# Optimization experiments

Hardware: AMD Instinct MI355X
Metric: run time of the kernel (lower is better)

Reference implementation:

```python
import jax, jax.numpy as jnp
import numpy as np

N_NODES = 100000
N_EDGES = 640000
NIN = 128
NOUT = 128


def setup_inputs() -> dict:
    key = jax.random.key(0)
    ks = jax.random.split(key, 10)
    scale = 1.0 / np.sqrt(NIN)
    x = jax.random.normal(ks[0], (N_NODES, NIN), dtype=jnp.float32)
    edge_index = jax.random.randint(ks[1], (2, N_EDGES), 0, N_NODES, dtype=jnp.int64)
    edge_attr = jnp.zeros((N_EDGES, 1), dtype=jnp.float32)
    Wk = jax.random.uniform(ks[2], (NIN, NOUT), jnp.float32, -scale, scale)
    bk = jax.random.uniform(ks[3], (NOUT,), jnp.float32, -scale, scale)
    Wq = jax.random.uniform(ks[4], (NIN, NOUT), jnp.float32, -scale, scale)
    bq = jax.random.uniform(ks[5], (NOUT,), jnp.float32, -scale, scale)
    Wv = jax.random.uniform(ks[6], (NIN, NOUT), jnp.float32, -scale, scale)
    bv = jax.random.uniform(ks[7], (NOUT,), jnp.float32, -scale, scale)
    Wskip = jax.random.uniform(ks[8], (NIN, NOUT), jnp.float32, -scale, scale)
    bias = jax.random.uniform(ks[9], (NOUT,), jnp.float32, -scale, scale)
    return {
        "x": x, "edge_index": edge_index, "edge_attr": edge_attr,
        "Wk": Wk, "bk": bk, "Wq": Wq, "bq": bq,
        "Wv": Wv, "bv": bv, "Wskip": Wskip, "bias": bias,
    }


def reference(x, edge_index, edge_attr, Wk, bk, Wq, bq, Wv, bv, Wskip, bias):
    # PyG ResGatedGraphConv: out_i = W_skip x_i + b + sum_{j->i} sigmoid(k_i + q_j) * v_j
    # k = lin_key(x) (applied to dst), q = lin_query(x) (src), v = lin_value(x) (src)
    src, dst = edge_index[0], edge_index[1]
    k = x @ Wk + bk            # [N, NOUT]
    q = x @ Wq + bq            # [N, NOUT]
    v = x @ Wv + bv            # [N, NOUT]
    eta = jax.nn.sigmoid(k[dst] + q[src])   # [E, NOUT] per-edge gate
    msg = eta * v[src]                       # [E, NOUT]
    agg = jax.ops.segment_sum(msg, dst, num_segments=x.shape[0])  # [N, NOUT]
    return agg + x @ Wskip + bias
```

## Files before the change

kernel.cpp:

```cpp
#include <hip/hip_runtime.h>
#include <hip/hip_bf16.h>

typedef __bf16 v4bf __attribute__((ext_vector_type(4)));
typedef __bf16 v8bf __attribute__((ext_vector_type(8)));
typedef float  v16f __attribute__((ext_vector_type(16)));

#define LOG2E 1.44269504088896340736f

__device__ __forceinline__ unsigned short f2bf(float f) {
    union { float f; unsigned int u; } a; a.f = f;
    unsigned int r = a.u + 0x7FFFu + ((a.u >> 16) & 1u);
    return (unsigned short)(r >> 16);
}

__device__ __forceinline__ void unpack8(uint4 rawv, float* f) {
    unsigned int w[4] = { rawv.x, rawv.y, rawv.z, rawv.w };
    #pragma unroll
    for (int i = 0; i < 4; ++i) {
        f[2 * i]     = __uint_as_float(w[i] << 16);
        f[2 * i + 1] = __uint_as_float(w[i] & 0xFFFF0000u);
    }
}

__global__ __launch_bounds__(256) void prep_w_zero(
    const float* __restrict__ Wk, const float* __restrict__ Wq,
    const float* __restrict__ Wv, const float* __restrict__ Ws,
    unsigned short* __restrict__ Wt, int* __restrict__ deg, int N)
{
    int i = blockIdx.x * 256 + threadIdx.x;
    if (i < 65536) {
        int m = i >> 14;
        int r = i & 16383;
        int n = r >> 7, k = r & 127;
        const float* W = (m == 0) ? Wk : (m == 1) ? Wq : (m == 2) ? Wv : Ws;
        float scale = (m < 2) ? LOG2E : 1.0f;
        Wt[i] = f2bf(W[k * 128 + n] * scale);
    }
    if (i < N) deg[i] = 0;
}

__global__ __launch_bounds__(1024, 4) void gemm_fused(
    const float* __restrict__ x, int N,
    const unsigned short* __restrict__ Wt,
    const float* __restrict__ bk, const float* __restrict__ bq,
    const float* __restrict__ bv, const float* __restrict__ bs,
    unsigned short* __restrict__ kws, unsigned short* __restrict__ qv,
    float* __restrict__ out)
{
    __shared__ __align__(16) unsigned short xs[32 * 132];
    const int t   = threadIdx.x;
    const int wid = t >> 6;
    const int m   = wid >> 2;
    const int ct  = wid & 3;
    const int l   = t & 63;
    const int col = ct * 32 + (l & 31);
    const int kb  = (l >> 5) * 8;

    v8bf b[8];
    {
        const unsigned short* wp = Wt + m * 16384 + col * 128 + kb;
        #pragma unroll
        for (int c = 0; c < 8; ++c) b[c] = *(const v8bf*)(wp + c * 16);
    }
    const float* bvec = (m == 0) ? bk : (m == 1) ? bq : (m == 2) ? bv : bs;
    const float bcol = bvec[col] * ((m < 2) ? LOG2E : 1.0f);
    unsigned short* dst; int dstride;
    if (m == 0)      { dst = kws;      dstride = 128; }
    else if (m == 1) { dst = qv;       dstride = 256; }
    else             { dst = qv + 128; dstride = 256; }

    const int srow = t >> 5;
    const int sk4  = (t & 31) << 2;
    const int rowb = 4 * (l >> 5);

    const int ntiles = (N + 31) >> 5;
    int tile = blockIdx.x;
    if (tile >= ntiles) return;

    float4 stg = make_float4(0.f, 0.f, 0.f, 0.f);
    {
        int gr = tile * 32 + srow;
        if (gr < N) stg = *(const float4*)(x + (size_t)gr * 128 + sk4);
    }

    const unsigned short* ap = xs + (l & 31) * 132 + kb;

    while (true) {
        ushort4 pk;
        pk.x = f2bf(stg.x); pk.y = f2bf(stg.y);
        pk.z = f2bf(stg.z); pk.w = f2bf(stg.w);
        *(ushort4*)(xs + srow * 132 + sk4) = pk;
        __syncthreads();

        int next = tile + gridDim.x;
        if (next < ntiles) {
            int gr = next * 32 + srow;
            stg = (gr < N) ? *(const float4*)(x + (size_t)gr * 128 + sk4)
                           : make_float4(0.f, 0.f, 0.f, 0.f);
        }

        v16f acc = {};
        #pragma unroll
        for (int c = 0; c < 8; ++c) {
            v4bf a0 = *(const v4bf*)(ap + c * 16);
            v4bf a1 = *(const v4bf*)(ap + c * 16 + 4);
            v8bf a = __builtin_shufflevector(a0, a1, 0, 1, 2, 3, 4, 5, 6, 7);
            acc = __builtin_amdgcn_mfma_f32_32x32x16_bf16(a, b[c], acc, 0, 0, 0);
        }

        const int r0 = tile * 32 + rowb;
        if (m == 3) {
            #pragma unroll
            for (int reg = 0; reg < 16; ++reg) {
                int row = r0 + (reg & 3) + 8 * (reg >> 2);
                if (row < N) out[(size_t)row * 128 + col] = acc[reg] + bcol;
            }
        } else {
            #pragma unroll
            for (int reg = 0; reg < 16; ++reg) {
                int row = r0 + (reg & 3) + 8 * (reg >> 2);
                if (row < N) dst[(size_t)row * dstride + col] = f2bf(acc[reg] + bcol);
            }
        }

        tile = next;
        if (tile >= ntiles) break;
        __syncthreads();
    }
}


__global__ __launch_bounds__(256) void count_deg(
    const int* __restrict__ ei, int E, int* __restrict__ deg)
{
    int e = blockIdx.x * 256 + threadIdx.x;
    if (e >= E) return;
    atomicAdd(&deg[ei[E + e]], 1);
}

__global__ __launch_bounds__(256) void scan_chunks(
    const int* __restrict__ deg, int N, int* __restrict__ rowStart,
    int* __restrict__ chunkTot)
{
    __shared__ int sums[256];
    const int t = threadIdx.x;
    const int base = blockIdx.x * 1024 + t * 4;
    int d0 = 0, d1 = 0, d2 = 0, d3 = 0;
    if (base + 3 < N) {
        int4 dd = *(const int4*)(deg + base);
        d0 = dd.x; d1 = dd.y; d2 = dd.z; d3 = dd.w;
    } else {
        if (base + 0 < N) d0 = deg[base + 0];
        if (base + 1 < N) d1 = deg[base + 1];
        if (base + 2 < N) d2 = deg[base + 2];
        if (base + 3 < N) d3 = deg[base + 3];
    }
    int tot = d0 + d1 + d2 + d3;
    sums[t] = tot;
    __syncthreads();
    #pragma unroll
    for (int off = 1; off < 256; off <<= 1) {
        int v = (t >= off) ? sums[t - off] : 0;
        __syncthreads();
        sums[t] += v;
        __syncthreads();
    }
    int excl = sums[t] - tot;
    if (base + 0 < N) rowStart[base + 0] = excl;
    if (base + 1 < N) rowStart[base + 1] = excl + d0;
    if (base + 2 < N) rowStart[base + 2] = excl + d0 + d1;
    if (base + 3 < N) rowStart[base + 3] = excl + d0 + d1 + d2;
    if (t == 255) chunkTot[blockIdx.x] = sums[255];
}

__global__ __launch_bounds__(256) void add_offsets(
    int* __restrict__ rowStart, int* __restrict__ rowEnd,
    const int* __restrict__ chunkTot, int N, int nChunks)
{
    __shared__ int s[128];
    const int t = threadIdx.x;
    if (t < 128) s[t] = (t < nChunks) ? chunkTot[t] : 0;
    __syncthreads();
    #pragma unroll
    for (int off = 1; off < 128; off <<= 1) {
        int u = 0;
        if (t < 128 && t >= off) u = s[t - off];
        __syncthreads();
        if (t < 128) s[t] += u;
        __syncthreads();
    }
    const int coff = (blockIdx.x == 0) ? 0 : s[blockIdx.x - 1];
    const int base = blockIdx.x * 1024 + t * 4;
    if (base + 3 < N) {
        int4 r = *(const int4*)(rowStart + base);
        r.x += coff; r.y += coff; r.z += coff; r.w += coff;
        *(int4*)(rowStart + base) = r;
        *(int4*)(rowEnd + base) = r;
    } else {
        #pragma unroll
        for (int j = 0; j < 4; ++j) {
            if (base + j < N) {
                int v = rowStart[base + j] + coff;
                rowStart[base + j] = v;
                rowEnd[base + j] = v;
            }
        }
    }
}

__global__ __launch_bounds__(256) void fill_csr(
    const int* __restrict__ ei, int E,
    int* __restrict__ rowEnd, int* __restrict__ elist)
{
    int e = blockIdx.x * 256 + threadIdx.x;
    if (e >= E) return;
    int s = ei[e];
    int d = ei[E + e];
    int pos = atomicAdd(&rowEnd[d], 1);
    elist[pos] = s;
}

__global__ __launch_bounds__(256) void gather_agg(
    const int* __restrict__ rowStart, const int* __restrict__ rowEnd,
    const int* __restrict__ elist,
    const unsigned short* __restrict__ kws,
    const unsigned short* __restrict__ qv,
    float* __restrict__ out, int N)
{
    int gid = blockIdx.x * 256 + threadIdx.x;
    int node = gid >> 4;
    if (node >= N) return;
    int fo = (gid & 15) << 3;

    uint4 kraw = *(const uint4*)(kws + (size_t)node * 128 + fo);
    kraw.x ^= 0x80008000u; kraw.y ^= 0x80008000u;
    kraw.z ^= 0x80008000u; kraw.w ^= 0x80008000u;
    float nkf[8];
    unpack8(kraw, nkf);
    float acc[8] = {};

    const unsigned short* qvb = qv + fo;
    int p = rowStart[node];
    const int e = rowEnd[node];

    for (; p + 4 <= e; p += 4) {
        int s0 = elist[p], s1 = elist[p + 1], s2 = elist[p + 2], s3 = elist[p + 3];
        const unsigned short* r0 = qvb + (size_t)s0 * 256;
        const unsigned short* r1 = qvb + (size_t)s1 * 256;
        const unsigned short* r2 = qvb + (size_t)s2 * 256;
        const unsigned short* r3 = qvb + (size_t)s3 * 256;
        uint4 q0r = *(const uint4*)(r0);
        uint4 v0r = *(const uint4*)(r0 + 128);
        uint4 q1r = *(const uint4*)(r1);
        uint4 v1r = *(const uint4*)(r1 + 128);
        uint4 q2r = *(const uint4*)(r2);
        uint4 v2r = *(const uint4*)(r2 + 128);
        uint4 q3r = *(const uint4*)(r3);
        uint4 v3r = *(const uint4*)(r3 + 128);
        float qf[8], vf[8];
        unpack8(q0r, qf); unpack8(v0r, vf);
        #pragma unroll
        for (int j = 0; j < 8; ++j) {
            float ex = __builtin_amdgcn_exp2f(nkf[j] - qf[j]);
            acc[j] = fmaf(__builtin_amdgcn_rcpf(1.0f + ex), vf[j], acc[j]);
        }
        unpack8(q1r, qf); unpack8(v1r, vf);
        #pragma unroll
        for (int j = 0; j < 8; ++j) {
            float ex = __builtin_amdgcn_exp2f(nkf[j] - qf[j]);
            acc[j] = fmaf(__builtin_amdgcn_rcpf(1.0f + ex), vf[j], acc[j]);
        }
        unpack8(q2r, qf); unpack8(v2r, vf);
        #pragma unroll
        for (int j = 0; j < 8; ++j) {
            float ex = __builtin_amdgcn_exp2f(nkf[j] - qf[j]);
            acc[j] = fmaf(__builtin_amdgcn_rcpf(1.0f + ex), vf[j], acc[j]);
        }
        unpack8(q3r, qf); unpack8(v3r, vf);
        #pragma unroll
        for (int j = 0; j < 8; ++j) {
            float ex = __builtin_amdgcn_exp2f(nkf[j] - qf[j]);
            acc[j] = fmaf(__builtin_amdgcn_rcpf(1.0f + ex), vf[j], acc[j]);
        }
    }
    for (; p < e; ++p) {
        int s0 = elist[p];
        const unsigned short* r0 = qvb + (size_t)s0 * 256;
        uint4 q0r = *(const uint4*)(r0);
        uint4 v0r = *(const uint4*)(r0 + 128);
        float qf[8], vf[8];
        unpack8(q0r, qf); unpack8(v0r, vf);
        #pragma unroll
        for (int j = 0; j < 8; ++j) {
            float ex = __builtin_amdgcn_exp2f(nkf[j] - qf[j]);
            acc[j] = fmaf(__builtin_amdgcn_rcpf(1.0f + ex), vf[j], acc[j]);
        }
    }

    float* orow = out + (size_t)node * 128 + fo;
    float4 o0 = *(float4*)(orow);
    float4 o1 = *(float4*)(orow + 4);
    o0.x += acc[0]; o0.y += acc[1]; o0.z += acc[2]; o0.w += acc[3];
    o1.x += acc[4]; o1.y += acc[5]; o1.z += acc[6]; o1.w += acc[7];
    *(float4*)(orow)     = o0;
    *(float4*)(orow + 4) = o1;
}

extern "C" void kernel_launch(void* const* d_in, const int* in_sizes, int n_in,
                              void* d_out, int out_size, void* d_ws, size_t ws_size,
                              hipStream_t stream) {
    const float* x    = (const float*)d_in[0];
    const int*   ei   = (const int*)d_in[1];
    const float* Wk   = (const float*)d_in[3];
    const float* bk   = (const float*)d_in[4];
    const float* Wq   = (const float*)d_in[5];
    const float* bq   = (const float*)d_in[6];
    const float* Wv   = (const float*)d_in[7];
    const float* bv   = (const float*)d_in[8];
    const float* Ws   = (const float*)d_in[9];
    const float* bias = (const float*)d_in[10];

    const int N = in_sizes[0] / 128;
    const int E = in_sizes[1] / 2;
    float* out = (float*)d_out;

    unsigned short* kws = (unsigned short*)d_ws;
    unsigned short* qv  = kws + (size_t)N * 128;
    int* deg      = (int*)(qv + (size_t)N * 256);
    int* rowStart = deg + N;
    int* rowEnd   = rowStart + N;
    int* chunkTot = rowEnd + N;
    int* elist    = chunkTot + 128;
    unsigned short* Wt = (unsigned short*)(elist + E);

    const int nChunks = (N + 1023) / 1024;

    prep_w_zero<<<512, 256, 0, stream>>>(Wk, Wq, Wv, Ws, Wt, deg, N);
    gemm_fused<<<1024, 1024, 0, stream>>>(
        x, N, Wt, bk, bq, bv, bias, kws, qv, out);

    count_deg<<<(E + 255) / 256, 256, 0, stream>>>(ei, E, deg);
    scan_chunks<<<nChunks, 256, 0, stream>>>(deg, N, rowStart, chunkTot);
    add_offsets<<<nChunks, 256, 0, stream>>>(rowStart, rowEnd, chunkTot, N, nChunks);
    fill_csr<<<(E + 255) / 256, 256, 0, stream>>>(ei, E, rowEnd, elist);

    gather_agg<<<((size_t)N * 16 + 255) / 256, 256, 0, stream>>>(
        rowStart, rowEnd, elist, kws, qv, out, N);
}
```

Measured before the change: 279.9 us.

## Record per-edge slot in degree pass, drop fill atomics, batch gather loads by 8

```diff
diff --git a/kernel.cpp b/kernel.cpp
--- a/kernel.cpp
+++ b/kernel.cpp
@@ -33,7 +33,7 @@
         int r = i & 16383;
         int n = r >> 7, k = r & 127;
         const float* W = (m == 0) ? Wk : (m == 1) ? Wq : (m == 2) ? Wv : Ws;
-        float scale = (m < 2) ? LOG2E : 1.0f;
+        float scale = (m == 0) ? -LOG2E : (m == 1) ? LOG2E : 1.0f;
         Wt[i] = f2bf(W[k * 128 + n] * scale);
     }
     if (i < N) deg[i] = 0;
@@ -63,7 +63,7 @@
         for (int c = 0; c < 8; ++c) b[c] = *(const v8bf*)(wp + c * 16);
     }
     const float* bvec = (m == 0) ? bk : (m == 1) ? bq : (m == 2) ? bv : bs;
-    const float bcol = bvec[col] * ((m < 2) ? LOG2E : 1.0f);
+    const float bcol = bvec[col] * ((m == 0) ? -LOG2E : (m == 1) ? LOG2E : 1.0f);
     unsigned short* dst; int dstride;
     if (m == 0)      { dst = kws;      dstride = 128; }
     else if (m == 1) { dst = qv;       dstride = 256; }
@@ -130,12 +130,13 @@
 }
 
 
-__global__ __launch_bounds__(256) void count_deg(
-    const int* __restrict__ ei, int E, int* __restrict__ deg)
+__global__ __launch_bounds__(256) void count_pos(
+    const int* __restrict__ ei, int E, int* __restrict__ deg,
+    int* __restrict__ pos)
 {
     int e = blockIdx.x * 256 + threadIdx.x;
     if (e >= E) return;
-    atomicAdd(&deg[ei[E + e]], 1);
+    pos[e] = atomicAdd(&deg[ei[E + e]], 1);
 }
 
 __global__ __launch_bounds__(256) void scan_chunks(
@@ -174,8 +175,8 @@
 }
 
 __global__ __launch_bounds__(256) void add_offsets(
-    int* __restrict__ rowStart, int* __restrict__ rowEnd,
-    const int* __restrict__ chunkTot, int N, int nChunks)
+    int* __restrict__ rowStart, const int* __restrict__ chunkTot,
+    int N, int nChunks)
 {
     __shared__ int s[128];
     const int t = threadIdx.x;
@@ -195,33 +196,28 @@
         int4 r = *(const int4*)(rowStart + base);
         r.x += coff; r.y += coff; r.z += coff; r.w += coff;
         *(int4*)(rowStart + base) = r;
-        *(int4*)(rowEnd + base) = r;
     } else {
         #pragma unroll
         for (int j = 0; j < 4; ++j) {
-            if (base + j < N) {
-                int v = rowStart[base + j] + coff;
-                rowStart[base + j] = v;
-                rowEnd[base + j] = v;
-            }
+            if (base + j < N) rowStart[base + j] += coff;
         }
     }
 }
 
 __global__ __launch_bounds__(256) void fill_csr(
     const int* __restrict__ ei, int E,
-    int* __restrict__ rowEnd, int* __restrict__ elist)
+    const int* __restrict__ rowStart, const int* __restrict__ pos,
+    int* __restrict__ elist)
 {
     int e = blockIdx.x * 256 + threadIdx.x;
     if (e >= E) return;
     int s = ei[e];
     int d = ei[E + e];
-    int pos = atomicAdd(&rowEnd[d], 1);
-    elist[pos] = s;
-}
-
-__global__ __launch_bounds__(256) void gather_agg(
-    const int* __restrict__ rowStart, const int* __restrict__ rowEnd,
+    elist[rowStart[d] + pos[e]] = s;
+}
+
+__global__ __launch_bounds__(256, 4) void gather_agg(
+    const int* __restrict__ rowStart, const int* __restrict__ deg,
     const int* __restrict__ elist,
     const unsigned short* __restrict__ kws,
     const unsigned short* __restrict__ qv,
@@ -232,74 +228,50 @@
     if (node >= N) return;
     int fo = (gid & 15) << 3;
 
+    float* orow = out + (size_t)node * 128 + fo;
+    float4 o0 = *(const float4*)(orow);
+    float4 o1 = *(const float4*)(orow + 4);
     uint4 kraw = *(const uint4*)(kws + (size_t)node * 128 + fo);
-    kraw.x ^= 0x80008000u; kraw.y ^= 0x80008000u;
-    kraw.z ^= 0x80008000u; kraw.w ^= 0x80008000u;
+    const int p0 = rowStart[node];
+    const int dg = deg[node];
+
     float nkf[8];
     unpack8(kraw, nkf);
     float acc[8] = {};
 
     const unsigned short* qvb = qv + fo;
-    int p = rowStart[node];
-    const int e = rowEnd[node];
-
-    for (; p + 4 <= e; p += 4) {
-        int s0 = elist[p], s1 = elist[p + 1], s2 = elist[p + 2], s3 = elist[p + 3];
-        const unsigned short* r0 = qvb + (size_t)s0 * 256;
-        const unsigned short* r1 = qvb + (size_t)s1 * 256;
-        const unsigned short* r2 = qvb + (size_t)s2 * 256;
-        const unsigned short* r3 = qvb + (size_t)s3 * 256;
-        uint4 q0r = *(const uint4*)(r0);
-        uint4 v0r = *(const uint4*)(r0 + 128);
-        uint4 q1r = *(const uint4*)(r1);
-        uint4 v1r = *(const uint4*)(r1 + 128);
-        uint4 q2r = *(const uint4*)(r2);
-        uint4 v2r = *(const uint4*)(r2 + 128);
-        uint4 q3r = *(const uint4*)(r3);
-        uint4 v3r = *(const uint4*)(r3 + 128);
-        float qf[8], vf[8];
-        unpack8(q0r, qf); unpack8(v0r, vf);
-        #pragma unroll
-        for (int j = 0; j < 8; ++j) {
-            float ex = __builtin_amdgcn_exp2f(nkf[j] - qf[j]);
-            acc[j] = fmaf(__builtin_amdgcn_rcpf(1.0f + ex), vf[j], acc[j]);
-        }
-        unpack8(q1r, qf); unpack8(v1r, vf);
-        #pragma unroll
-        for (int j = 0; j < 8; ++j) {
-            float ex = __builtin_amdgcn_exp2f(nkf[j] - qf[j]);
-            acc[j] = fmaf(__builtin_amdgcn_rcpf(1.0f + ex), vf[j], acc[j]);
-        }
-        unpack8(q2r, qf); unpack8(v2r, vf);
-        #pragma unroll
-        for (int j = 0; j < 8; ++j) {
-            float ex = __builtin_amdgcn_exp2f(nkf[j] - qf[j]);
-            acc[j] = fmaf(__builtin_amdgcn_rcpf(1.0f + ex), vf[j], acc[j]);
-        }
-        unpack8(q3r, qf); unpack8(v3r, vf);
-        #pragma unroll
-        for (int j = 0; j < 8; ++j) {
-            float ex = __builtin_amdgcn_exp2f(nkf[j] - qf[j]);
-            acc[j] = fmaf(__builtin_amdgcn_rcpf(1.0f + ex), vf[j], acc[j]);
-        }
-    }
-    for (; p < e; ++p) {
-        int s0 = elist[p];
-        const unsigned short* r0 = qvb + (size_t)s0 * 256;
-        uint4 q0r = *(const uint4*)(r0);
-        uint4 v0r = *(const uint4*)(r0 + 128);
-        float qf[8], vf[8];
-        unpack8(q0r, qf); unpack8(v0r, vf);
-        #pragma unroll
-        for (int j = 0; j < 8; ++j) {
-            float ex = __builtin_amdgcn_exp2f(nkf[j] - qf[j]);
-            acc[j] = fmaf(__builtin_amdgcn_rcpf(1.0f + ex), vf[j], acc[j]);
-        }
-    }
-
-    float* orow = out + (size_t)node * 128 + fo;
-    float4 o0 = *(float4*)(orow);
-    float4 o1 = *(float4*)(orow + 4);
+    const int e = p0 + dg;
+
+    for (int base = p0; base < e; base += 8) {
+        int idx[8];
+        #pragma unroll
+        for (int s = 0; s < 8; ++s) {
+            int pp = base + s;
+            idx[s] = elist[pp < e ? pp : e - 1];
+        }
+        uint4 qr[8], vr[8];
+        #pragma unroll
+        for (int s = 0; s < 8; ++s) {
+            const unsigned short* r = qvb + (idx[s] << 8);
+            qr[s] = *(const uint4*)(r);
+            vr[s] = *(const uint4*)(r + 128);
+        }
+        #pragma unroll
+        for (int s = 0; s < 8; ++s) {
+            if (base + s >= e) {
+                vr[s].x = 0u; vr[s].y = 0u; vr[s].z = 0u; vr[s].w = 0u;
+            }
+            float qf[8], vf[8];
+            unpack8(qr[s], qf);
+            unpack8(vr[s], vf);
+            #pragma unroll
+            for (int j = 0; j < 8; ++j) {
+                float ex = __builtin_amdgcn_exp2f(nkf[j] - qf[j]);
+                acc[j] = fmaf(__builtin_amdgcn_rcpf(1.0f + ex), vf[j], acc[j]);
+            }
+        }
+    }
+
     o0.x += acc[0]; o0.y += acc[1]; o0.z += acc[2]; o0.w += acc[3];
     o1.x += acc[4]; o1.y += acc[5]; o1.z += acc[6]; o1.w += acc[7];
     *(float4*)(orow)     = o0;
@@ -328,9 +300,9 @@
     unsigned short* qv  = kws + (size_t)N * 128;
     int* deg      = (int*)(qv + (size_t)N * 256);
     int* rowStart = deg + N;
-    int* rowEnd   = rowStart + N;
-    int* chunkTot = rowEnd + N;
-    int* elist    = chunkTot + 128;
+    int* chunkTot = rowStart + N;
+    int* pos      = chunkTot + 128;
+    int* elist    = pos + E;
     unsigned short* Wt = (unsigned short*)(elist + E);
 
     const int nChunks = (N + 1023) / 1024;
@@ -339,11 +311,11 @@
     gemm_fused<<<1024, 1024, 0, stream>>>(
         x, N, Wt, bk, bq, bv, bias, kws, qv, out);
 
-    count_deg<<<(E + 255) / 256, 256, 0, stream>>>(ei, E, deg);
+    count_pos<<<(E + 255) / 256, 256, 0, stream>>>(ei, E, deg, pos);
     scan_chunks<<<nChunks, 256, 0, stream>>>(deg, N, rowStart, chunkTot);
-    add_offsets<<<nChunks, 256, 0, stream>>>(rowStart, rowEnd, chunkTot, N, nChunks);
-    fill_csr<<<(E + 255) / 256, 256, 0, stream>>>(ei, E, rowEnd, elist);
+    add_offsets<<<nChunks, 256, 0, stream>>>(rowStart, chunkTot, N, nChunks);
+    fill_csr<<<(E + 255) / 256, 256, 0, stream>>>(ei, E, rowStart, pos, elist);
 
     gather_agg<<<((size_t)N * 16 + 255) / 256, 256, 0, stream>>>(
-        rowStart, rowEnd, elist, kws, qv, out, N);
-}
+        rowStart, deg, elist, kws, qv, out, N);
+}
```

After: 268.9 us. -3.9%, faster.
